# Kernel tuning notes

Measured on AMD Instinct MI355X. Metric: run time of the kernel, lower is better.

## Reference

```python
import jax, jax.numpy as jnp
import numpy as np

N_USER, N_VIDEO, N_PUB, N_TAG = 200000, 100000, 20000, 5000
EMB = 128
HALF = EMB // 2
LAYER_NUM = 3


def setup_inputs() -> dict:
    key = jax.random.key(0)
    ks = jax.random.split(key, 20)
    inp = {
        "user_emb": jax.random.normal(ks[0], (N_USER, EMB), jnp.float32),
        "video_emb": jax.random.normal(ks[1], (N_VIDEO, EMB), jnp.float32),
        "publisher_emb": jax.random.normal(ks[2], (N_PUB, EMB), jnp.float32),
        "tag_emb": jax.random.normal(ks[3], (N_TAG, EMB), jnp.float32),
    }
    # (name, E, n_src, n_dst)
    rels = [
        ("uv", 1500000, N_USER, N_VIDEO),
        ("vu", 1500000, N_VIDEO, N_USER),
        ("up", 800000, N_USER, N_PUB),
        ("pu", 800000, N_PUB, N_USER),
        ("vt", 800000, N_VIDEO, N_TAG),
        ("tv", 800000, N_TAG, N_VIDEO),
        ("pt", 400000, N_PUB, N_TAG),
        ("tp", 400000, N_TAG, N_PUB),
    ]
    for i, (name, E, ns, nd) in enumerate(rels):
        inp[name + "_src"] = jax.random.randint(ks[4 + 2 * i], (E,), 0, ns, jnp.int32)
        inp[name + "_dst"] = jax.random.randint(ks[5 + 2 * i], (E,), 0, nd, jnp.int32)
    return inp


def _seg_mean(feat, src, dst, num_dst):
    # copy_u + mean: gather half-dim src features, segment-mean onto dst.
    msg = feat[src]                                             # [E, HALF]
    s = jax.ops.segment_sum(msg, dst, num_segments=num_dst)     # [num_dst, HALF]
    deg = jax.ops.segment_sum(jnp.ones_like(dst, dtype=feat.dtype), dst,
                              num_segments=num_dst)
    return s / jnp.maximum(deg, 1.0)[:, None]  # zero-in-degree nodes -> 0 (DGL behavior)


def reference(user_emb, video_emb, publisher_emb, tag_emb,
              uv_src, uv_dst, vu_src, vu_dst,
              up_src, up_dst, pu_src, pu_dst,
              vt_src, vt_dst, tv_src, tv_dst,
              pt_src, pt_dst, tp_src, tp_dst):

    def layer(u, v, p, t):
        # user dst: [vu, pu]; video dst: [uv, tv]; publisher dst: [up, tp]; tag dst: [vt, pt]
        vu = _seg_mean(v[:, :HALF], vu_src, vu_dst, N_USER)
        pu = _seg_mean(p[:, :HALF], pu_src, pu_dst, N_USER)
        uv = _seg_mean(u[:, :HALF], uv_src, uv_dst, N_VIDEO)
        tv = _seg_mean(t[:, :HALF], tv_src, tv_dst, N_VIDEO)
        up = _seg_mean(u[:, HALF:], up_src, up_dst, N_PUB)
        tp = _seg_mean(t[:, HALF:], tp_src, tp_dst, N_PUB)
        vt = _seg_mean(v[:, HALF:], vt_src, vt_dst, N_TAG)
        pt = _seg_mean(p[:, HALF:], pt_src, pt_dst, N_TAG)
        return (jnp.concatenate([vu, pu], axis=1),
                jnp.concatenate([uv, tv], axis=1),
                jnp.concatenate([up, tp], axis=1),
                jnp.concatenate([vt, pt], axis=1))

    pu_, pv_, pp_, pt_ = user_emb, video_emb, publisher_emb, tag_emb
    u, v, p, t = user_emb, video_emb, publisher_emb, tag_emb
    for i in range(LAYER_NUM):
        u, v, p, t = layer(u, v, p, t)
        w = 1.0 / (i + 2)
        pu_ = pu_ + u * w
        pv_ = pv_ + v * w
        pp_ = pp_ + p * w
        pt_ = pt_ + t * w
    return (pu_, pv_, pp_, pt_)
```

## Files before the change

kernel.cpp:

```cpp
#include <hip/hip_runtime.h>
#include <hip/hip_bf16.h>
#include <stdint.h>

#define EMB 128
#define CAP 12288

static constexpr int N_USER = 200000, N_VIDEO = 100000, N_PUB = 20000, N_TAG = 5000;
static constexpr int ROW_U = 0, ROW_V = 200000, ROW_P = 300000, ROW_T = 320000;
static constexpr int ROWS = 325000;
static constexpr int TOTAL_E = 7000000;
static constexpr int TOTAL_GROUPS = 650000;
static constexpr int TILE = 8192;

__device__ inline unsigned bf16_rne(float f) {
  unsigned u = __float_as_uint(f);
  return (u + 0x7fffu + ((u >> 16) & 1u)) >> 16;
}
__device__ inline unsigned pack_bf16x2(float lo, float hi) {
  return bf16_rne(lo) | (bf16_rne(hi) << 16);
}

struct SortDesc {
  int tcum[9];
  int bcum[9];
  int gcum[8];
  int E[8];
  int n_dst[8];
  int wshift[8];
  const int* esrc[8];
  const int* edst[8];
};

struct AggrDesc {
  int cum[9];
  int src_base[8];
  int src_col[8];
  int dst_base[8];
  int dst_col[8];
  const float* demb[8];
};

__global__ __launch_bounds__(256) void part_kernel(SortDesc d, unsigned* __restrict__ pairs,
                                                   int* __restrict__ cursors) {
  __shared__ int cnt[256];
  __shared__ int lcur[256];
  int blk = blockIdx.x;
  int r = 0;
#pragma unroll
  for (int k = 1; k < 8; ++k) if (blk >= d.tcum[k]) r = k;
  int base = (blk - d.tcum[r]) * TILE;
  int n = min(TILE, d.E[r] - base);
  const int* __restrict__ esrc = d.esrc[r];
  const int* __restrict__ edst = d.edst[r];
  int tid = threadIdx.x;
  int B = d.bcum[r + 1] - d.bcum[r];
  int sh = d.wshift[r];
  int msk = (1 << sh) - 1;
  int bb = d.bcum[r];
  if (tid < B) cnt[tid] = 0;
  __syncthreads();
  for (int i = tid; i < n; i += 256)
    atomicAdd(&cnt[edst[base + i] >> sh], 1);
  __syncthreads();
  if (tid < B) {
    int c = cnt[tid];
    lcur[tid] = c ? atomicAdd(&cursors[bb + tid], c) : 0;
  }
  __syncthreads();
  for (int i = tid; i < n; i += 256) {
    int dv = edst[base + i];
    int sv = esrc[base + i];
    int b = dv >> sh;
    int pos = atomicAdd(&lcur[b], 1);
    if (pos < CAP)
      pairs[(size_t)(bb + b) * CAP + pos] = ((unsigned)(dv & msk) << 18) | (unsigned)sv;
  }
}

__global__ __launch_bounds__(256) void bases_kernel(const int* __restrict__ cursors,
                                                    int* __restrict__ bases, int NB) {
  __shared__ int wsums[4];
  int tid = threadIdx.x;
  int L = (NB + 255) / 256;
  int lo = min(tid * L, NB), hi = min(lo + L, NB);
  int s = 0;
  for (int i = lo; i < hi; ++i) s += cursors[i];
  int lane = tid & 63, wv = tid >> 6;
  int v = s;
#pragma unroll
  for (int dd = 1; dd < 64; dd <<= 1) {
    int t = __shfl_up(v, dd);
    if (lane >= dd) v += t;
  }
  if (lane == 63) wsums[wv] = v;
  __syncthreads();
  if (tid == 0) {
    int run = 0;
#pragma unroll
    for (int k = 0; k < 4; ++k) { int t = wsums[k]; wsums[k] = run; run += t; }
  }
  __syncthreads();
  int run = wsums[wv] + (v - s);
  for (int i = lo; i < hi; ++i) { int c = cursors[i]; bases[i] = run; run += c; }
}

__global__ __launch_bounds__(256) void build_kernel(SortDesc d, const unsigned* __restrict__ pairs,
                                                    const int* __restrict__ cursors,
                                                    const int* __restrict__ bases,
                                                    int* __restrict__ sorted,
                                                    int* __restrict__ Beg, int* __restrict__ Deg) {
  __shared__ int cnt[1024];
  __shared__ int stage[CAP];
  __shared__ int wsums[4];
  int bucket = blockIdx.x;
  int r = 0;
#pragma unroll
  for (int k = 1; k < 8; ++k) if (bucket >= d.bcum[k]) r = k;
  int bl = bucket - d.bcum[r];
  int sh = d.wshift[r];
  int first = bl << sh;
  int Wa = min(1 << sh, d.n_dst[r] - first);
  int tid = threadIdx.x;
  int n_b = min(cursors[bucket], CAP);
  int gbase = bases[bucket];
  const unsigned* __restrict__ bp = pairs + (size_t)bucket * CAP;

  for (int i = tid; i < 1024; i += 256) cnt[i] = 0;
  __syncthreads();
  for (int i = tid; i < n_b; i += 256)
    atomicAdd(&cnt[bp[i] >> 18], 1);
  __syncthreads();

  int t4 = tid * 4;
  int c0 = cnt[t4], c1 = cnt[t4 + 1], c2 = cnt[t4 + 2], c3 = cnt[t4 + 3];
  int s = c0 + c1 + c2 + c3;
  int lane = tid & 63, wv = tid >> 6;
  int v = s;
#pragma unroll
  for (int dd = 1; dd < 64; dd <<= 1) {
    int t = __shfl_up(v, dd);
    if (lane >= dd) v += t;
  }
  if (lane == 63) wsums[wv] = v;
  __syncthreads();
  if (tid == 0) {
    int run = 0;
#pragma unroll
    for (int k = 0; k < 4; ++k) { int t = wsums[k]; wsums[k] = run; run += t; }
  }
  __syncthreads();
  int ex = wsums[wv] + (v - s);
  int o0 = ex, o1 = ex + c0, o2 = o1 + c1, o3 = o2 + c2;
  cnt[t4] = o0; cnt[t4 + 1] = o1; cnt[t4 + 2] = o2; cnt[t4 + 3] = o3;
  int g0 = d.gcum[r] + first + t4;
  if (t4 + 0 < Wa) { Beg[g0 + 0] = gbase + o0; Deg[g0 + 0] = c0; }
  if (t4 + 1 < Wa) { Beg[g0 + 1] = gbase + o1; Deg[g0 + 1] = c1; }
  if (t4 + 2 < Wa) { Beg[g0 + 2] = gbase + o2; Deg[g0 + 2] = c2; }
  if (t4 + 3 < Wa) { Beg[g0 + 3] = gbase + o3; Deg[g0 + 3] = c3; }
  __syncthreads();

  for (int i = tid; i < n_b; i += 256) {
    unsigned pr = bp[i];
    int pos = atomicAdd(&cnt[pr >> 18], 1);
    stage[pos] = (int)(pr & 0x3FFFFu);
  }
  __syncthreads();
  for (int i = tid; i < n_b; i += 256)
    sorted[gbase + i] = stage[i];
}

__global__ void convert_kernel(const float* __restrict__ u, const float* __restrict__ v,
                               const float* __restrict__ p, const float* __restrict__ t,
                               uint16_t* __restrict__ feat) {
  int idx = blockIdx.x * blockDim.x + threadIdx.x;
  const int total8 = ROWS * EMB / 8;
  if (idx >= total8) return;
  int flat = idx * 8;
  int row = flat >> 7;
  int col = flat & 127;
  const float* s;
  if (row < ROW_V)      s = u + (size_t)row * EMB + col;
  else if (row < ROW_P) s = v + (size_t)(row - ROW_V) * EMB + col;
  else if (row < ROW_T) s = p + (size_t)(row - ROW_P) * EMB + col;
  else                  s = t + (size_t)(row - ROW_T) * EMB + col;
  float4 f0 = *(const float4*)s;
  float4 f1 = *((const float4*)s + 1);
  uint4 o;
  o.x = pack_bf16x2(f0.x, f0.y);
  o.y = pack_bf16x2(f0.z, f0.w);
  o.z = pack_bf16x2(f1.x, f1.y);
  o.w = pack_bf16x2(f1.z, f1.w);
  *(uint4*)(feat + flat) = o;
}

#define ACC(q) \
  a0 += __uint_as_float((q).x << 16); a1 += __uint_as_float((q).x & 0xffff0000u); \
  a2 += __uint_as_float((q).y << 16); a3 += __uint_as_float((q).y & 0xffff0000u); \
  a4 += __uint_as_float((q).z << 16); a5 += __uint_as_float((q).z & 0xffff0000u); \
  a6 += __uint_as_float((q).w << 16); a7 += __uint_as_float((q).w & 0xffff0000u);

__global__ __launch_bounds__(256) void aggr_kernel(AggrDesc d, const uint16_t* __restrict__ prev,
                                                   uint16_t* __restrict__ next,
                                                   float* __restrict__ out, int mode,
                                                   const int* __restrict__ sorted,
                                                   const int* __restrict__ Beg,
                                                   const int* __restrict__ Deg) {
  int g = blockIdx.x * 32 + (threadIdx.x >> 3);
  if (g >= TOTAL_GROUPS) return;
  int lane = threadIdx.x & 7;
  int r = 0;
#pragma unroll
  for (int k = 1; k < 8; ++k) if (g >= d.cum[k]) r = k;
  int n = g - d.cum[r];
  int beg = Beg[g], dg = Deg[g];
  float recip = 1.0f / (float)(dg > 0 ? dg : 1);
  const uint16_t* sbase = prev + (size_t)d.src_base[r] * EMB + d.src_col[r] + lane * 8;
  float a0 = 0.f, a1 = 0.f, a2 = 0.f, a3 = 0.f, a4 = 0.f, a5 = 0.f, a6 = 0.f, a7 = 0.f;
  int e = beg, end = beg + dg;
  while (e + 8 <= end) {
    int myi = sorted[e + lane];
    uint4 q[8];
#pragma unroll
    for (int j = 0; j < 8; ++j) {
      int sj = __shfl(myi, j, 8);
      q[j] = *(const uint4*)(sbase + (size_t)sj * EMB);
    }
#pragma unroll
    for (int j = 0; j < 8; ++j) { ACC(q[j]); }
    e += 8;
  }
  int rem = end - e;
  if (rem > 0) {
    int myi = sorted[e + (lane < rem ? lane : 0)];
    uint4 q[7];
#pragma unroll
    for (int j = 0; j < 7; ++j) {
      if (j < rem) {
        int sj = __shfl(myi, j, 8);
        q[j] = *(const uint4*)(sbase + (size_t)sj * EMB);
      }
    }
#pragma unroll
    for (int j = 0; j < 7; ++j) {
      if (j < rem) { ACC(q[j]); }
    }
  }
  a0 *= recip; a1 *= recip; a2 *= recip; a3 *= recip;
  a4 *= recip; a5 *= recip; a6 *= recip; a7 *= recip;

  int col = d.dst_col[r] + lane * 8;
  size_t dpos = (size_t)(d.dst_base[r] + n) * EMB + col;

  if (mode == 0) {
    uint4 ov;
    ov.x = pack_bf16x2(a0, a1);
    ov.y = pack_bf16x2(a2, a3);
    ov.z = pack_bf16x2(a4, a5);
    ov.w = pack_bf16x2(a6, a7);
    *(uint4*)(next + dpos) = ov;
    return;
  }

  uint4 q1 = *(const uint4*)(next + dpos);
  uint4 q2 = *(const uint4*)(prev + dpos);
  const float* de = d.demb[r] + (size_t)n * EMB + col;
  float4 v0 = *(const float4*)de;
  float4 v1 = *((const float4*)de + 1);
  const float w1 = 0.5f, w2 = 1.0f / 3.0f, w3 = 0.25f;
  v0.x += w1 * __uint_as_float(q1.x << 16)         + w2 * __uint_as_float(q2.x << 16)         + w3 * a0;
  v0.y += w1 * __uint_as_float(q1.x & 0xffff0000u) + w2 * __uint_as_float(q2.x & 0xffff0000u) + w3 * a1;
  v0.z += w1 * __uint_as_float(q1.y << 16)         + w2 * __uint_as_float(q2.y << 16)         + w3 * a2;
  v0.w += w1 * __uint_as_float(q1.y & 0xffff0000u) + w2 * __uint_as_float(q2.y & 0xffff0000u) + w3 * a3;
  v1.x += w1 * __uint_as_float(q1.z << 16)         + w2 * __uint_as_float(q2.z << 16)         + w3 * a4;
  v1.y += w1 * __uint_as_float(q1.z & 0xffff0000u) + w2 * __uint_as_float(q2.z & 0xffff0000u) + w3 * a5;
  v1.z += w1 * __uint_as_float(q1.w << 16)         + w2 * __uint_as_float(q2.w << 16)         + w3 * a6;
  v1.w += w1 * __uint_as_float(q1.w & 0xffff0000u) + w2 * __uint_as_float(q2.w & 0xffff0000u) + w3 * a7;
  *(float4*)(out + dpos) = v0;
  *((float4*)(out + dpos) + 1) = v1;
}

extern "C" void kernel_launch(void* const* d_in, const int* in_sizes, int n_in,
                              void* d_out, int out_size, void* d_ws, size_t ws_size,
                              hipStream_t stream) {
  const float* emb_u = (const float*)d_in[0];
  const float* emb_v = (const float*)d_in[1];
  const float* emb_p = (const float*)d_in[2];
  const float* emb_t = (const float*)d_in[3];

  struct RelInfo { int si, di, E, n_dst, src_base, src_col, dst_base, dst_col, wshift; };
  const RelInfo rels[8] = {
    {12, 13,  800000, N_TAG,   ROW_V, 64, ROW_T,  0,  5},
    {16, 17,  400000, N_TAG,   ROW_P, 64, ROW_T, 64,  5},
    { 8,  9,  800000, N_PUB,   ROW_U, 64, ROW_P,  0,  7},
    {18, 19,  400000, N_PUB,   ROW_T, 64, ROW_P, 64,  7},
    { 4,  5, 1500000, N_VIDEO, ROW_U,  0, ROW_V,  0,  9},
    {14, 15,  800000, N_VIDEO, ROW_T,  0, ROW_V, 64,  9},
    { 6,  7, 1500000, N_USER,  ROW_V,  0, ROW_U,  0, 10},
    {10, 11,  800000, N_USER,  ROW_P,  0, ROW_U, 64, 10},
  };
  const float* dembs[8] = {emb_t, emb_t, emb_p, emb_p, emb_v, emb_v, emb_u, emb_u};

  char* ws = (char*)d_ws;
  size_t cursor = 0;
  auto take = [&](size_t bytes) -> char* {
    char* p = ws + cursor;
    cursor = (cursor + bytes + 255) & ~(size_t)255;
    return p;
  };
  uint16_t* featA = (uint16_t*)take((size_t)ROWS * EMB * 2);
  uint16_t* featB = (uint16_t*)take((size_t)ROWS * EMB * 2);
  int* sorted = (int*)take((size_t)TOTAL_E * 4);
  int* Beg    = (int*)take((size_t)TOTAL_GROUPS * 4);
  int* Deg    = (int*)take((size_t)TOTAL_GROUPS * 4);
  unsigned* pairs = (unsigned*)d_ws;

  SortDesc sd;
  AggrDesc ad;
  int tacc = 0, bacc = 0, gacc = 0;
  for (int r = 0; r < 8; ++r) {
    int n_dst = rels[r].n_dst;
    sd.tcum[r] = tacc; tacc += (rels[r].E + TILE - 1) / TILE;
    sd.bcum[r] = bacc; bacc += (n_dst + (1 << rels[r].wshift) - 1) >> rels[r].wshift;
    sd.gcum[r] = gacc;
    sd.E[r] = rels[r].E;
    sd.n_dst[r] = n_dst;
    sd.wshift[r] = rels[r].wshift;
    sd.esrc[r] = (const int*)d_in[rels[r].si];
    sd.edst[r] = (const int*)d_in[rels[r].di];

    ad.cum[r] = gacc;
    ad.src_base[r] = rels[r].src_base;
    ad.src_col[r] = rels[r].src_col;
    ad.dst_base[r] = rels[r].dst_base;
    ad.dst_col[r] = rels[r].dst_col;
    ad.demb[r] = dembs[r];
    gacc += n_dst;
  }
  sd.tcum[8] = tacc;
  sd.bcum[8] = bacc;
  ad.cum[8] = gacc;

  int* cursors = (int*)take((size_t)bacc * 4);
  int* bases   = (int*)take((size_t)bacc * 4);

  hipMemsetAsync(cursors, 0, (size_t)bacc * 4, stream);
  part_kernel<<<tacc, 256, 0, stream>>>(sd, pairs, cursors);
  bases_kernel<<<1, 256, 0, stream>>>(cursors, bases, bacc);
  build_kernel<<<bacc, 256, 0, stream>>>(sd, pairs, cursors, bases, sorted, Beg, Deg);

  convert_kernel<<<(ROWS * EMB / 8 + 255) / 256, 256, 0, stream>>>(emb_u, emb_v, emb_p, emb_t, featA);

  float* out = (float*)d_out;
  const int aggr_blocks = (TOTAL_GROUPS + 31) / 32;
  aggr_kernel<<<aggr_blocks, 256, 0, stream>>>(ad, featA, featB, out, 0, sorted, Beg, Deg);
  aggr_kernel<<<aggr_blocks, 256, 0, stream>>>(ad, featB, featA, out, 0, sorted, Beg, Deg);
  aggr_kernel<<<aggr_blocks, 256, 0, stream>>>(ad, featA, featB, out, 1, sorted, Beg, Deg);
}
```

Baseline: 618.8 us.

## Pad CSR segments to multiples of 8 with zero row; drop bases scan kernel

Each destination's edge list is padded to a multiple of 8 using a sentinel source index that points to an all-zero feature row, so the aggregation loop has no remainder path and can prefetch the next chunk's indices. Bucket base offsets are now claimed with a global atomic counter inside the build kernel, which removes the separate single-block scan launch. The epilogue uses nontemporal loads and stores for streamed data, and a scheduling barrier groups the gathers ahead of the accumulations. The cost is extra padded gathers of the zero row, a larger sorted buffer and shared-memory stage, and a CSR layout whose bucket order is no longer deterministic.

```diff
diff --git a/kernel.cpp b/kernel.cpp
--- a/kernel.cpp
+++ b/kernel.cpp
@@ -1,9 +1,9 @@
 #include <hip/hip_runtime.h>
-#include <hip/hip_bf16.h>
 #include <stdint.h>
 
 #define EMB 128
-#define CAP 12288
+#define PCAP 12288
+#define SCAP 13312
 
 static constexpr int N_USER = 200000, N_VIDEO = 100000, N_PUB = 20000, N_TAG = 5000;
 static constexpr int ROW_U = 0, ROW_V = 200000, ROW_P = 300000, ROW_T = 320000;
@@ -11,6 +11,10 @@
 static constexpr int TOTAL_E = 7000000;
 static constexpr int TOTAL_GROUPS = 650000;
 static constexpr int TILE = 8192;
+static constexpr int SORT_MAX = TOTAL_E + 7 * TOTAL_GROUPS;
+
+using f32x4 = __attribute__((ext_vector_type(4))) float;
+using u32x4 = __attribute__((ext_vector_type(4))) unsigned int;
 
 __device__ inline unsigned bf16_rne(float f) {
   unsigned u = __float_as_uint(f);
@@ -27,6 +31,7 @@
   int E[8];
   int n_dst[8];
   int wshift[8];
+  int zrow[8];
   const int* esrc[8];
   const int* edst[8];
 };
@@ -72,46 +77,21 @@
     int sv = esrc[base + i];
     int b = dv >> sh;
     int pos = atomicAdd(&lcur[b], 1);
-    if (pos < CAP)
-      pairs[(size_t)(bb + b) * CAP + pos] = ((unsigned)(dv & msk) << 18) | (unsigned)sv;
-  }
-}
-
-__global__ __launch_bounds__(256) void bases_kernel(const int* __restrict__ cursors,
-                                                    int* __restrict__ bases, int NB) {
-  __shared__ int wsums[4];
-  int tid = threadIdx.x;
-  int L = (NB + 255) / 256;
-  int lo = min(tid * L, NB), hi = min(lo + L, NB);
-  int s = 0;
-  for (int i = lo; i < hi; ++i) s += cursors[i];
-  int lane = tid & 63, wv = tid >> 6;
-  int v = s;
-#pragma unroll
-  for (int dd = 1; dd < 64; dd <<= 1) {
-    int t = __shfl_up(v, dd);
-    if (lane >= dd) v += t;
-  }
-  if (lane == 63) wsums[wv] = v;
-  __syncthreads();
-  if (tid == 0) {
-    int run = 0;
-#pragma unroll
-    for (int k = 0; k < 4; ++k) { int t = wsums[k]; wsums[k] = run; run += t; }
-  }
-  __syncthreads();
-  int run = wsums[wv] + (v - s);
-  for (int i = lo; i < hi; ++i) { int c = cursors[i]; bases[i] = run; run += c; }
+    if (pos < PCAP)
+      pairs[(size_t)(bb + b) * PCAP + pos] = ((unsigned)(dv & msk) << 18) | (unsigned)sv;
+  }
 }
 
 __global__ __launch_bounds__(256) void build_kernel(SortDesc d, const unsigned* __restrict__ pairs,
                                                     const int* __restrict__ cursors,
-                                                    const int* __restrict__ bases,
+                                                    int* __restrict__ gcounter,
                                                     int* __restrict__ sorted,
                                                     int* __restrict__ Beg, int* __restrict__ Deg) {
   __shared__ int cnt[1024];
-  __shared__ int stage[CAP];
+  __shared__ int poff[1025];
+  __shared__ int stage[SCAP];
   __shared__ int wsums[4];
+  __shared__ int sh_gbase;
   int bucket = blockIdx.x;
   int r = 0;
 #pragma unroll
@@ -120,10 +100,10 @@
   int sh = d.wshift[r];
   int first = bl << sh;
   int Wa = min(1 << sh, d.n_dst[r] - first);
+  int zr = d.zrow[r];
   int tid = threadIdx.x;
-  int n_b = min(cursors[bucket], CAP);
-  int gbase = bases[bucket];
-  const unsigned* __restrict__ bp = pairs + (size_t)bucket * CAP;
+  int n_b = min(cursors[bucket], PCAP);
+  const unsigned* __restrict__ bp = pairs + (size_t)bucket * PCAP;
 
   for (int i = tid; i < 1024; i += 256) cnt[i] = 0;
   __syncthreads();
@@ -133,7 +113,8 @@
 
   int t4 = tid * 4;
   int c0 = cnt[t4], c1 = cnt[t4 + 1], c2 = cnt[t4 + 2], c3 = cnt[t4 + 3];
-  int s = c0 + c1 + c2 + c3;
+  int p0 = (c0 + 7) & ~7, p1 = (c1 + 7) & ~7, p2 = (c2 + 7) & ~7, p3 = (c3 + 7) & ~7;
+  int s = p0 + p1 + p2 + p3;
   int lane = tid & 63, wv = tid >> 6;
   int v = s;
 #pragma unroll
@@ -150,8 +131,16 @@
   }
   __syncthreads();
   int ex = wsums[wv] + (v - s);
-  int o0 = ex, o1 = ex + c0, o2 = o1 + c1, o3 = o2 + c2;
+  if (tid == 255) {
+    int tot = ex + s;
+    sh_gbase = atomicAdd(gcounter, tot);
+    poff[1024] = min(tot, SCAP);
+  }
+  __syncthreads();
+  int gbase = sh_gbase;
+  int o0 = ex, o1 = ex + p0, o2 = o1 + p1, o3 = o2 + p2;
   cnt[t4] = o0; cnt[t4 + 1] = o1; cnt[t4 + 2] = o2; cnt[t4 + 3] = o3;
+  poff[t4] = o0; poff[t4 + 1] = o1; poff[t4 + 2] = o2; poff[t4 + 3] = o3;
   int g0 = d.gcum[r] + first + t4;
   if (t4 + 0 < Wa) { Beg[g0 + 0] = gbase + o0; Deg[g0 + 0] = c0; }
   if (t4 + 1 < Wa) { Beg[g0 + 1] = gbase + o1; Deg[g0 + 1] = c1; }
@@ -162,21 +151,37 @@
   for (int i = tid; i < n_b; i += 256) {
     unsigned pr = bp[i];
     int pos = atomicAdd(&cnt[pr >> 18], 1);
-    stage[pos] = (int)(pr & 0x3FFFFu);
-  }
-  __syncthreads();
-  for (int i = tid; i < n_b; i += 256)
+    if (pos < SCAP) stage[pos] = (int)(pr & 0x3FFFFu);
+  }
+  __syncthreads();
+
+#pragma unroll
+  for (int jj = 0; jj < 4; ++jj) {
+    int j = t4 + jj;
+    int end_ = min((j < 1023) ? poff[j + 1] : poff[1024], SCAP);
+    for (int k = cnt[j]; k < end_; ++k) stage[k] = zr;
+  }
+  __syncthreads();
+
+  int tot = poff[1024];
+  for (int i = tid; i < tot; i += 256)
     sorted[gbase + i] = stage[i];
 }
 
 __global__ void convert_kernel(const float* __restrict__ u, const float* __restrict__ v,
                                const float* __restrict__ p, const float* __restrict__ t,
-                               uint16_t* __restrict__ feat) {
+                               uint16_t* __restrict__ featA, uint16_t* __restrict__ featB) {
   int idx = blockIdx.x * blockDim.x + threadIdx.x;
-  const int total8 = ROWS * EMB / 8;
+  const int total8 = (ROWS + 1) * EMB / 8;
   if (idx >= total8) return;
   int flat = idx * 8;
   int row = flat >> 7;
+  if (row == ROWS) {
+    uint4 z = {0u, 0u, 0u, 0u};
+    *(uint4*)(featA + flat) = z;
+    *(uint4*)(featB + flat) = z;
+    return;
+  }
   int col = flat & 127;
   const float* s;
   if (row < ROW_V)      s = u + (size_t)row * EMB + col;
@@ -190,7 +195,7 @@
   o.y = pack_bf16x2(f0.z, f0.w);
   o.z = pack_bf16x2(f1.x, f1.y);
   o.w = pack_bf16x2(f1.z, f1.w);
-  *(uint4*)(feat + flat) = o;
+  *(uint4*)(featA + flat) = o;
 }
 
 #define ACC(q) \
@@ -214,36 +219,29 @@
   int n = g - d.cum[r];
   int beg = Beg[g], dg = Deg[g];
   float recip = 1.0f / (float)(dg > 0 ? dg : 1);
-  const uint16_t* sbase = prev + (size_t)d.src_base[r] * EMB + d.src_col[r] + lane * 8;
+  const uint16_t* __restrict__ sbase = prev + (size_t)d.src_base[r] * EMB + d.src_col[r] + lane * 8;
   float a0 = 0.f, a1 = 0.f, a2 = 0.f, a3 = 0.f, a4 = 0.f, a5 = 0.f, a6 = 0.f, a7 = 0.f;
-  int e = beg, end = beg + dg;
-  while (e + 8 <= end) {
-    int myi = sorted[e + lane];
-    uint4 q[8];
-#pragma unroll
-    for (int j = 0; j < 8; ++j) {
-      int sj = __shfl(myi, j, 8);
-      q[j] = *(const uint4*)(sbase + (size_t)sj * EMB);
-    }
-#pragma unroll
-    for (int j = 0; j < 8; ++j) { ACC(q[j]); }
-    e += 8;
-  }
-  int rem = end - e;
-  if (rem > 0) {
-    int myi = sorted[e + (lane < rem ? lane : 0)];
-    uint4 q[7];
-#pragma unroll
-    for (int j = 0; j < 7; ++j) {
-      if (j < rem) {
-        int sj = __shfl(myi, j, 8);
-        q[j] = *(const uint4*)(sbase + (size_t)sj * EMB);
-      }
-    }
-#pragma unroll
-    for (int j = 0; j < 7; ++j) {
-      if (j < rem) { ACC(q[j]); }
-    }
+  int nchunk = (dg + 7) >> 3;
+  int e = beg + lane;
+  int myi = (nchunk > 0) ? sorted[e] : 0;
+  for (int c = 0; c < nchunk; ++c) {
+    int nyi = (c + 1 < nchunk) ? sorted[e + 8] : 0;
+    int s0 = __shfl(myi, 0, 8), s1 = __shfl(myi, 1, 8);
+    int s2 = __shfl(myi, 2, 8), s3 = __shfl(myi, 3, 8);
+    int s4 = __shfl(myi, 4, 8), s5 = __shfl(myi, 5, 8);
+    int s6 = __shfl(myi, 6, 8), s7 = __shfl(myi, 7, 8);
+    uint4 q0 = *(const uint4*)(sbase + (size_t)s0 * EMB);
+    uint4 q1 = *(const uint4*)(sbase + (size_t)s1 * EMB);
+    uint4 q2 = *(const uint4*)(sbase + (size_t)s2 * EMB);
+    uint4 q3 = *(const uint4*)(sbase + (size_t)s3 * EMB);
+    uint4 q4 = *(const uint4*)(sbase + (size_t)s4 * EMB);
+    uint4 q5 = *(const uint4*)(sbase + (size_t)s5 * EMB);
+    uint4 q6 = *(const uint4*)(sbase + (size_t)s6 * EMB);
+    uint4 q7 = *(const uint4*)(sbase + (size_t)s7 * EMB);
+    __builtin_amdgcn_sched_barrier(0);
+    ACC(q0); ACC(q1); ACC(q2); ACC(q3);
+    ACC(q4); ACC(q5); ACC(q6); ACC(q7);
+    myi = nyi; e += 8;
   }
   a0 *= recip; a1 *= recip; a2 *= recip; a3 *= recip;
   a4 *= recip; a5 *= recip; a6 *= recip; a7 *= recip;
@@ -261,11 +259,11 @@
     return;
   }
 
-  uint4 q1 = *(const uint4*)(next + dpos);
+  u32x4 q1 = __builtin_nontemporal_load((const u32x4*)(next + dpos));
   uint4 q2 = *(const uint4*)(prev + dpos);
-  const float* de = d.demb[r] + (size_t)n * EMB + col;
-  float4 v0 = *(const float4*)de;
-  float4 v1 = *((const float4*)de + 1);
+  const f32x4* de = (const f32x4*)(d.demb[r] + (size_t)n * EMB + col);
+  f32x4 v0 = __builtin_nontemporal_load(de);
+  f32x4 v1 = __builtin_nontemporal_load(de + 1);
   const float w1 = 0.5f, w2 = 1.0f / 3.0f, w3 = 0.25f;
   v0.x += w1 * __uint_as_float(q1.x << 16)         + w2 * __uint_as_float(q2.x << 16)         + w3 * a0;
   v0.y += w1 * __uint_as_float(q1.x & 0xffff0000u) + w2 * __uint_as_float(q2.x & 0xffff0000u) + w3 * a1;
@@ -275,8 +273,8 @@
   v1.y += w1 * __uint_as_float(q1.z & 0xffff0000u) + w2 * __uint_as_float(q2.z & 0xffff0000u) + w3 * a5;
   v1.z += w1 * __uint_as_float(q1.w << 16)         + w2 * __uint_as_float(q2.w << 16)         + w3 * a6;
   v1.w += w1 * __uint_as_float(q1.w & 0xffff0000u) + w2 * __uint_as_float(q2.w & 0xffff0000u) + w3 * a7;
-  *(float4*)(out + dpos) = v0;
-  *((float4*)(out + dpos) + 1) = v1;
+  __builtin_nontemporal_store(v0, (f32x4*)(out + dpos));
+  __builtin_nontemporal_store(v1, (f32x4*)(out + dpos) + 1);
 }
 
 extern "C" void kernel_launch(void* const* d_in, const int* in_sizes, int n_in,
@@ -307,9 +305,9 @@
     cursor = (cursor + bytes + 255) & ~(size_t)255;
     return p;
   };
-  uint16_t* featA = (uint16_t*)take((size_t)ROWS * EMB * 2);
-  uint16_t* featB = (uint16_t*)take((size_t)ROWS * EMB * 2);
-  int* sorted = (int*)take((size_t)TOTAL_E * 4);
+  uint16_t* featA = (uint16_t*)take((size_t)(ROWS + 1) * EMB * 2);
+  uint16_t* featB = (uint16_t*)take((size_t)(ROWS + 1) * EMB * 2);
+  int* sorted = (int*)take((size_t)SORT_MAX * 4);
   int* Beg    = (int*)take((size_t)TOTAL_GROUPS * 4);
   int* Deg    = (int*)take((size_t)TOTAL_GROUPS * 4);
   unsigned* pairs = (unsigned*)d_ws;
@@ -325,6 +323,7 @@
     sd.E[r] = rels[r].E;
     sd.n_dst[r] = n_dst;
     sd.wshift[r] = rels[r].wshift;
+    sd.zrow[r] = ROWS - rels[r].src_base;
     sd.esrc[r] = (const int*)d_in[rels[r].si];
     sd.edst[r] = (const int*)d_in[rels[r].di];
 
@@ -340,15 +339,15 @@
   sd.bcum[8] = bacc;
   ad.cum[8] = gacc;
 
-  int* cursors = (int*)take((size_t)bacc * 4);
-  int* bases   = (int*)take((size_t)bacc * 4);
-
-  hipMemsetAsync(cursors, 0, (size_t)bacc * 4, stream);
+  int* cursors  = (int*)take((size_t)bacc * 4 + 4);
+  int* gcounter = cursors + bacc;
+
+  hipMemsetAsync(cursors, 0, (size_t)(bacc + 1) * 4, stream);
   part_kernel<<<tacc, 256, 0, stream>>>(sd, pairs, cursors);
-  bases_kernel<<<1, 256, 0, stream>>>(cursors, bases, bacc);
-  build_kernel<<<bacc, 256, 0, stream>>>(sd, pairs, cursors, bases, sorted, Beg, Deg);
-
-  convert_kernel<<<(ROWS * EMB / 8 + 255) / 256, 256, 0, stream>>>(emb_u, emb_v, emb_p, emb_t, featA);
+  build_kernel<<<bacc, 256, 0, stream>>>(sd, pairs, cursors, gcounter, sorted, Beg, Deg);
+
+  convert_kernel<<<((ROWS + 1) * EMB / 8 + 255) / 256, 256, 0, stream>>>(
+      emb_u, emb_v, emb_p, emb_t, featA, featB);
 
   float* out = (float*)d_out;
   const int aggr_blocks = (TOTAL_GROUPS + 31) / 32;
```

After: 617.5 us. No clear change (-0.2%).
